# Optimization experiments

Hardware: AMD Instinct MI355X
Metric: run time of the kernel (lower is better)

The kernel has to match this reference:

```python
import jax, jax.numpy as jnp
import numpy as np

N, E, IN, H, C = 100_000, 1_600_000, 128, 4, 32  # nodes, edges, in_dim, heads, per-head channels
HC = H * C
SLOPE = 0.2  # negative_slope


def setup_inputs() -> dict:
    key = jax.random.key(0)
    ks = jax.random.split(key, 20)
    rn = lambda k, shape, s=0.05: jax.random.normal(k, shape, jnp.float32) * s
    inp = {
        'x': rn(ks[0], (N, IN), 1.0),
        'edge_index': jax.random.randint(ks[1], (2, E), 0, N),
    }
    for i in range(3):
        din = IN if i == 0 else HC
        inp[f'W{i}'] = rn(ks[2 + 4 * i], (din, HC))
        inp[f'as{i}'] = rn(ks[3 + 4 * i], (H, C))
        inp[f'ad{i}'] = rn(ks[4 + 4 * i], (H, C))
        inp[f'b{i}'] = jnp.zeros((HC,), jnp.float32)
    inp['llW'] = rn(ks[14], (HC, HC))
    inp['llb'] = jnp.zeros((HC,), jnp.float32)
    inp['opW'] = rn(ks[15], (3 * HC, C))  # concat_dim=384 -> out_dim=32
    inp['opb'] = jnp.zeros((C,), jnp.float32)
    return inp


def gat_layer(h, src, dst, W, a_s, a_d, b):
    # PyG GATConv with concat=True, add_self_loops=False, edge_dim=None, eval-mode dropout
    xh = (h @ W).reshape(-1, H, C)                        # [N,H,C]
    e_src = (xh * a_s).sum(-1)                            # [N,H]
    e_dst = (xh * a_d).sum(-1)                            # [N,H]
    e = jax.nn.leaky_relu(e_src[src] + e_dst[dst], SLOPE)  # [E,H]
    emax = jax.ops.segment_max(e, dst, num_segments=N)    # segment softmax over dst
    ee = jnp.exp(e - emax[dst])
    denom = jax.ops.segment_sum(ee, dst, num_segments=N)
    alpha = ee / denom[dst]                               # [E,H]
    out = jax.ops.segment_sum(xh[src] * alpha[:, :, None], dst, num_segments=N)  # [N,H,C]
    return out.reshape(-1, HC) + b


def reference(x, edge_index, W0, as0, ad0, b0, W1, as1, ad1, b1, W2, as2, ad2, b2, llW, llb, opW, opb):
    src, dst = edge_index[0], edge_index[1]
    # layer 0 (no residual at layer 0)
    h0 = gat_layer(x, src, dst, W0, as0, ad0, b0)
    # layer 1: residual
    h1 = gat_layer(h0, src, dst, W1, as1, ad1, b1) + h0
    # layer 2: residual through last_linear
    h2 = gat_layer(h1, src, dst, W2, as2, ad2, b2) + (h1 @ llW + llb)
    # encoder head: concat hidden list, project
    h = jnp.concatenate([h0, h1, h2], axis=-1)  # [N, 384]
    return h @ opW + opb                         # [N, 32]
```

## Files before the change

### kernel.cpp

```cpp
#include <hip/hip_runtime.h>
#include <hip/hip_bf16.h>

#define NN  100000
#define NE  1600000
#define NH4 400000
#define NHC 12800000
#define NBLK 391
#define SC_CHUNK 2048
#define SC_NCHUNK ((NE + SC_CHUNK - 1) / SC_CHUNK)

typedef __attribute__((ext_vector_type(8))) short bf16x8;
typedef __attribute__((ext_vector_type(4))) float f32x4;

__device__ __forceinline__ ushort f2bf(float f) {
  uint u = __float_as_uint(f);
  u += 0x7fff + ((u >> 16) & 1);
  return (ushort)(u >> 16);
}
__device__ __forceinline__ uint pack2(float a, float b) {
  return (uint)f2bf(a) | ((uint)f2bf(b) << 16);
}
__device__ __forceinline__ float blo(uint u) { return __uint_as_float(u << 16); }
__device__ __forceinline__ float bhi(uint u) { return __uint_as_float(u & 0xffff0000u); }

__device__ __forceinline__ void stage_A_bf16(const uint* __restrict__ Ab, int row0,
                                             uint* __restrict__ As, int tid) {
  const uint4* __restrict__ Ag = (const uint4*)(Ab + (size_t)row0 * 64);
#pragma unroll
  for (int i = 0; i < 4; i++) {
    const int idx = tid + 512 * i;
    const int r = idx >> 4, c4 = idx & 15;
    uint4 v = make_uint4(0u, 0u, 0u, 0u);
    if (row0 + r < NN) v = Ag[idx];
    const uint off = (uint)(r * 64 + c4 * 4) ^ (uint)((r & 7) << 2);
    *(uint4*)&As[off] = v;
  }
}
__device__ __forceinline__ void stage_A_f32(const float* __restrict__ Af, int row0,
                                            uint* __restrict__ As, int tid) {
  const float4* __restrict__ Ag = (const float4*)(Af + (size_t)row0 * 128);
#pragma unroll
  for (int i = 0; i < 8; i++) {
    const int idx = tid + 512 * i;
    const int r = idx >> 5, k4 = idx & 31;
    float4 a = make_float4(0.f, 0.f, 0.f, 0.f);
    if (row0 + r < NN) a = Ag[idx];
    uint2 p;
    p.x = pack2(a.x, a.y);
    p.y = pack2(a.z, a.w);
    const uint off = (uint)(r * 64 + k4 * 2) ^ (uint)((r & 7) << 2);
    *(uint2*)&As[off] = p;
  }
}
__device__ __forceinline__ void stage_W(const float* __restrict__ W,
                                        uint* __restrict__ Wt, int tid) {
#pragma unroll
  for (int i = 0; i < 4; i++) {
    const int cid = tid + 512 * i;
    const int n = cid & 127;
    const int k8 = cid >> 7;
    float v[8];
#pragma unroll
    for (int j = 0; j < 8; j++) v[j] = W[(size_t)(k8 * 8 + j) * 128 + n];
    uint4 p;
    p.x = pack2(v[0], v[1]);
    p.y = pack2(v[2], v[3]);
    p.z = pack2(v[4], v[5]);
    p.w = pack2(v[6], v[7]);
    const uint off = (uint)(n * 64 + k8 * 4) ^ (uint)((n & 7) << 2);
    *(uint4*)&Wt[off] = p;
  }
}
__device__ __forceinline__ void load_afrag(const uint* __restrict__ As, int w, int l,
                                           bf16x8* afrag) {
  const int lrow = l & 15, lku = (l >> 4) * 4;
#pragma unroll
  for (int kc = 0; kc < 4; kc++) {
    const int r = w * 16 + lrow;
    const uint off = (uint)(r * 64 + lku + kc * 16) ^ (uint)((r & 7) << 2);
    afrag[kc] = *(const bf16x8*)&As[off];
  }
}

__device__ __forceinline__ void mfma_write(const uint* __restrict__ Wt,
                                           const bf16x8* afrag, int row0, int w, int l,
                                           const float* __restrict__ bias1,
                                           const float* __restrict__ bias2,
                                           ushort* __restrict__ out,
                                           const float* __restrict__ as_,
                                           const float* __restrict__ ad_,
                                           float* __restrict__ es,
                                           float* __restrict__ ed) {
  const int lrow = l & 15, lku = (l >> 4) * 4;
  const int r0 = row0 + w * 16 + (l >> 4) * 4;
#pragma unroll
  for (int pair = 0; pair < 4; pair++) {
    float pa[4] = {0.f, 0.f, 0.f, 0.f};
    float qa[4] = {0.f, 0.f, 0.f, 0.f};
#pragma unroll
    for (int sub = 0; sub < 2; sub++) {
      const int nt = pair * 2 + sub;
      const int n = nt * 16 + lrow;
      f32x4 acc = {0.f, 0.f, 0.f, 0.f};
#pragma unroll
      for (int kc = 0; kc < 4; kc++) {
        const uint off = (uint)(n * 64 + lku + kc * 16) ^ (uint)((n & 7) << 2);
        const bf16x8 bfrag = *(const bf16x8*)&Wt[off];
        acc = __builtin_amdgcn_mfma_f32_16x16x32_bf16(afrag[kc], bfrag, acc, 0, 0, 0);
      }
      float badd = 0.f;
      if (bias1) badd += bias1[n];
      if (bias2) badd += bias2[n];
#pragma unroll
      for (int reg = 0; reg < 4; reg++) {
        const int r = r0 + reg;
        if (r < NN) out[(size_t)r * 128 + n] = f2bf(acc[reg] + badd);
      }
      if (as_) {
        const float av = as_[n], dv = ad_[n];
#pragma unroll
        for (int reg = 0; reg < 4; reg++) {
          pa[reg] = fmaf(acc[reg], av, pa[reg]);
          qa[reg] = fmaf(acc[reg], dv, qa[reg]);
        }
      }
    }
    if (as_) {
#pragma unroll
      for (int m = 1; m <= 8; m <<= 1) {
#pragma unroll
        for (int reg = 0; reg < 4; reg++) {
          pa[reg] += __shfl_xor(pa[reg], m);
          qa[reg] += __shfl_xor(qa[reg], m);
        }
      }
      if (lrow == 0) {
#pragma unroll
        for (int reg = 0; reg < 4; reg++) {
          const int r = r0 + reg;
          if (r < NN) {
            es[r * 4 + pair] = pa[reg];
            ed[r * 4 + pair] = qa[reg];
          }
        }
      }
    }
  }
}

template <bool ABF16>
__global__ __launch_bounds__(512) void gemm128_k(const void* __restrict__ Av,
                                                 const float* __restrict__ W,
                                                 ushort* __restrict__ out,
                                                 const float* __restrict__ bias1,
                                                 const float* __restrict__ bias2,
                                                 const float* __restrict__ as_,
                                                 const float* __restrict__ ad_,
                                                 float* __restrict__ es,
                                                 float* __restrict__ ed) {
  __shared__ uint As[128 * 64];
  __shared__ uint Wt[128 * 64];
  const int tid = threadIdx.x;
  const int row0 = blockIdx.x * 128;
  if constexpr (ABF16) stage_A_bf16((const uint*)Av, row0, As, tid);
  else                 stage_A_f32((const float*)Av, row0, As, tid);
  stage_W(W, Wt, tid);
  __syncthreads();
  const int w = tid >> 6, l = tid & 63;
  bf16x8 afrag[4];
  load_afrag(As, w, l, afrag);
  mfma_write(Wt, afrag, row0, w, l, bias1, bias2, out, as_, ad_, es, ed);
}

__global__ __launch_bounds__(512) void gemm2_k(const uint* __restrict__ Ab,
                                               const float* __restrict__ W1,
                                               const float* __restrict__ b1a,
                                               const float* __restrict__ b1b,
                                               ushort* __restrict__ out1,
                                               const float* __restrict__ W2,
                                               ushort* __restrict__ out2,
                                               const float* __restrict__ as_,
                                               const float* __restrict__ ad_,
                                               float* __restrict__ es,
                                               float* __restrict__ ed) {
  __shared__ uint As[128 * 64];
  __shared__ uint Wt[128 * 64];
  const int tid = threadIdx.x;
  const int row0 = blockIdx.x * 128;
  stage_A_bf16(Ab, row0, As, tid);
  stage_W(W1, Wt, tid);
  __syncthreads();
  const int w = tid >> 6, l = tid & 63;
  bf16x8 afrag[4];
  load_afrag(As, w, l, afrag);
  mfma_write(Wt, afrag, row0, w, l, b1a, b1b, out1, nullptr, nullptr, nullptr, nullptr);
  __syncthreads();
  stage_W(W2, Wt, tid);
  __syncthreads();
  mfma_write(Wt, afrag, row0, w, l, nullptr, nullptr, out2, as_, ad_, es, ed);
}

__global__ __launch_bounds__(256) void hist_k(const int* __restrict__ dst, int* __restrict__ counts) {
  const int g = blockIdx.x & 7;
  const int chunk = blockIdx.x >> 3;
  const int lo = g * (NN / 8);
  const int hi = lo + (NN / 8);
  const int e0 = chunk * SC_CHUNK;
  const int e1 = (e0 + SC_CHUNK < NE) ? e0 + SC_CHUNK : NE;
  for (int i = e0 + threadIdx.x; i < e1; i += 256) {
    const int d = dst[i];
    if (d >= lo && d < hi) atomicAdd(&counts[d], 1);
  }
}

__global__ __launch_bounds__(256) void scan_blk_k(const int* __restrict__ counts,
                                                  int* __restrict__ row_start,
                                                  int* __restrict__ blocksum) {
  __shared__ int sm[256];
  const int t = threadIdx.x;
  const int i = blockIdx.x * 256 + t;
  const int c = (i < NN) ? counts[i] : 0;
  sm[t] = c;
  __syncthreads();
#pragma unroll
  for (int off = 1; off < 256; off <<= 1) {
    const int v = (t >= off) ? sm[t - off] : 0;
    __syncthreads();
    sm[t] += v;
    __syncthreads();
  }
  if (i < NN) row_start[i] = sm[t] - c;
  if (t == 255) blocksum[blockIdx.x] = sm[255];
}

__global__ __launch_bounds__(512) void scan_top_k(const int* __restrict__ blocksum,
                                                  int* __restrict__ blockoff) {
  __shared__ int sm[512];
  const int t = threadIdx.x;
  const int c = (t < NBLK) ? blocksum[t] : 0;
  sm[t] = c;
  __syncthreads();
#pragma unroll
  for (int off = 1; off < 512; off <<= 1) {
    const int v = (t >= off) ? sm[t - off] : 0;
    __syncthreads();
    sm[t] += v;
    __syncthreads();
  }
  if (t < NBLK) blockoff[t] = sm[t] - c;
}

__global__ __launch_bounds__(256) void scan_fix_k(int* __restrict__ row_start,
                                                  const int* __restrict__ blockoff,
                                                  int* __restrict__ cursor) {
  const int i = blockIdx.x * 256 + threadIdx.x;
  if (i < NN) {
    const int v = row_start[i] + blockoff[blockIdx.x];
    row_start[i] = v;
    cursor[i] = v;
  }
  if (i == 0) row_start[NN] = NE;
}

__global__ __launch_bounds__(256) void scatter_k(const int* __restrict__ src,
                                                 const int* __restrict__ dst,
                                                 int* __restrict__ cursor,
                                                 int* __restrict__ csr_src) {
  const int g = blockIdx.x & 7;
  const int chunk = blockIdx.x >> 3;
  const int lo = g * (NN / 8);
  const int hi = lo + (NN / 8);
  const int e0 = chunk * SC_CHUNK;
  const int e1 = (e0 + SC_CHUNK < NE) ? e0 + SC_CHUNK : NE;
  for (int i = e0 + threadIdx.x; i < e1; i += 256) {
    const int d = dst[i];
    if (d >= lo && d < hi) {
      const int pos = atomicAdd(&cursor[d], 1);
      csr_src[pos] = src[i];
    }
  }
}

#define EDGE_BODY(sv)                                                      \
  {                                                                        \
    const int s_ = (sv);                                                   \
    float v_ = es[s_ * 4 + h] + edh;                                       \
    v_ = v_ > 0.f ? v_ : 0.2f * v_;                                        \
    const float w_ = __expf(v_);                                           \
    const uint m_ = xbf[(size_t)s_ * 64 + l];                              \
    den += w_;                                                             \
    ax = fmaf(w_, blo(m_), ax);                                            \
    ay = fmaf(w_, bhi(m_), ay);                                            \
  }

__global__ __launch_bounds__(256) void gat_agg_k(const int* __restrict__ row_start,
                                                 const int* __restrict__ csr_src,
                                                 const float* __restrict__ es,
                                                 const float* __restrict__ ed,
                                                 const uint* __restrict__ xbf,
                                                 const ushort* __restrict__ base,
                                                 const float* __restrict__ bias,
                                                 ushort* __restrict__ out) {
  const int wid = (blockIdx.x * 256 + threadIdx.x) >> 6;
  if (wid >= NN) return;
  const int l = threadIdx.x & 63;
  const int h = l >> 4;
  const float edh = ed[wid * 4 + h];
  const int beg = row_start[wid], end = row_start[wid + 1];
  float ax = 0.f, ay = 0.f, den = 0.f;
  int i = beg;
  for (; i + 8 <= end; i += 8) {
    const int s0 = csr_src[i],     s1 = csr_src[i + 1];
    const int s2 = csr_src[i + 2], s3 = csr_src[i + 3];
    const int s4 = csr_src[i + 4], s5 = csr_src[i + 5];
    const int s6 = csr_src[i + 6], s7 = csr_src[i + 7];
    EDGE_BODY(s0) EDGE_BODY(s1) EDGE_BODY(s2) EDGE_BODY(s3)
    EDGE_BODY(s4) EDGE_BODY(s5) EDGE_BODY(s6) EDGE_BODY(s7)
  }
  for (; i + 4 <= end; i += 4) {
    const int s0 = csr_src[i],     s1 = csr_src[i + 1];
    const int s2 = csr_src[i + 2], s3 = csr_src[i + 3];
    EDGE_BODY(s0) EDGE_BODY(s1) EDGE_BODY(s2) EDGE_BODY(s3)
  }
  for (; i < end; i++) EDGE_BODY(csr_src[i]);

  const float inv = den > 0.f ? 1.f / den : 0.f;
  float rx = ax * inv, ry = ay * inv;
  const size_t o = (size_t)wid * 64 + l;
  if (base) {
    const uint b = ((const uint*)base)[o];
    rx += blo(b); ry += bhi(b);
  }
  if (bias) { rx += bias[l * 2]; ry += bias[l * 2 + 1]; }
  ((uint*)out)[o] = pack2(rx, ry);
}

__global__ __launch_bounds__(512) void out_proj_k(const uint* __restrict__ h0,
                                                  const uint* __restrict__ h1,
                                                  const uint* __restrict__ h2,
                                                  const float* __restrict__ opW,
                                                  const float* __restrict__ opb,
                                                  float* __restrict__ out) {
  __shared__ uint As[128 * 64];
  __shared__ uint Wt[32 * 192];
  const int tid = threadIdx.x;
  const int row0 = blockIdx.x * 128;

#pragma unroll
  for (int i = 0; i < 3; i++) {
    const int cid = tid + 512 * i;
    const int n = cid & 31;
    const int k8 = cid >> 5;
    float v[8];
#pragma unroll
    for (int j = 0; j < 8; j++) v[j] = opW[(size_t)(k8 * 8 + j) * 32 + n];
    uint4 p;
    p.x = pack2(v[0], v[1]);
    p.y = pack2(v[2], v[3]);
    p.z = pack2(v[4], v[5]);
    p.w = pack2(v[6], v[7]);
    const uint off = (uint)(n * 192 + k8 * 4) ^ (uint)((n & 7) << 2);
    *(uint4*)&Wt[off] = p;
  }

  const int w = tid >> 6, l = tid & 63;
  const int lrow = l & 15, lku = (l >> 4) * 4;
  f32x4 acc0 = {0.f, 0.f, 0.f, 0.f};
  f32x4 acc1 = {0.f, 0.f, 0.f, 0.f};
  const uint* __restrict__ hs[3] = {h0, h1, h2};

  for (int seg = 0; seg < 3; seg++) {
    __syncthreads();
    stage_A_bf16(hs[seg], row0, As, tid);
    __syncthreads();
    bf16x8 afrag[4];
    load_afrag(As, w, l, afrag);
#pragma unroll
    for (int kc = 0; kc < 4; kc++) {
      const int n0 = lrow, n1 = 16 + lrow;
      const uint off0 = (uint)(n0 * 192 + seg * 64 + lku + kc * 16) ^ (uint)((n0 & 7) << 2);
      const uint off1 = (uint)(n1 * 192 + seg * 64 + lku + kc * 16) ^ (uint)((n1 & 7) << 2);
      const bf16x8 b0 = *(const bf16x8*)&Wt[off0];
      const bf16x8 b1 = *(const bf16x8*)&Wt[off1];
      acc0 = __builtin_amdgcn_mfma_f32_16x16x32_bf16(afrag[kc], b0, acc0, 0, 0, 0);
      acc1 = __builtin_amdgcn_mfma_f32_16x16x32_bf16(afrag[kc], b1, acc1, 0, 0, 0);
    }
  }

  const int r0 = row0 + w * 16 + (l >> 4) * 4;
  const float ba = opb[lrow], bb = opb[16 + lrow];
#pragma unroll
  for (int reg = 0; reg < 4; reg++) {
    const int r = r0 + reg;
    if (r < NN) {
      out[(size_t)r * 32 + lrow]      = acc0[reg] + ba;
      out[(size_t)r * 32 + 16 + lrow] = acc1[reg] + bb;
    }
  }
}

extern "C" void kernel_launch(void* const* d_in, const int* in_sizes, int n_in,
                              void* d_out, int out_size, void* d_ws, size_t ws_size,
                              hipStream_t stream) {
  (void)in_sizes; (void)n_in; (void)out_size; (void)ws_size;
  const float* x  = (const float*)d_in[0];
  const int*   ei = (const int*)d_in[1];
  const int*  src = ei;
  const int*  dst = ei + NE;
  const float *W0 = (const float*)d_in[2],  *as0 = (const float*)d_in[3],
              *ad0 = (const float*)d_in[4], *b0 = (const float*)d_in[5];
  const float *W1 = (const float*)d_in[6],  *as1 = (const float*)d_in[7],
              *ad1 = (const float*)d_in[8], *b1 = (const float*)d_in[9];
  const float *W2 = (const float*)d_in[10], *as2 = (const float*)d_in[11],
              *ad2 = (const float*)d_in[12], *b2 = (const float*)d_in[13];
  const float *llW = (const float*)d_in[14], *llb = (const float*)d_in[15];
  const float *opW = (const float*)d_in[16], *opb = (const float*)d_in[17];

  char* w = (char*)d_ws;
  ushort* h0b = (ushort*)w; w += (size_t)NHC * 2;
  ushort* h1b = (ushort*)w; w += (size_t)NHC * 2;
  ushort* h2b = (ushort*)w; w += (size_t)NHC * 2;
  uint*   xbf = (uint*)w;   w += (size_t)NHC * 2;
  float*  es  = (float*)w;  w += (size_t)NH4 * 4;
  float*  ed  = (float*)w;  w += (size_t)NH4 * 4;
  int* row_start = (int*)w; w += (size_t)(NN + 1) * 4;
  int* cursor    = (int*)w; w += (size_t)NN * 4;
  int* counts    = (int*)w; w += (size_t)NN * 4;
  int* csr_src   = (int*)w; w += (size_t)NE * 4;
  int* blocksum  = (int*)w; w += (size_t)NBLK * 4;
  int* blockoff  = (int*)w;

  const dim3 blk(256);
  hipMemsetAsync(counts, 0, (size_t)NN * 4, stream);
  hist_k<<<SC_NCHUNK * 8, blk, 0, stream>>>(dst, counts);
  scan_blk_k<<<NBLK, blk, 0, stream>>>(counts, row_start, blocksum);
  scan_top_k<<<1, 512, 0, stream>>>(blocksum, blockoff);
  scan_fix_k<<<NBLK, blk, 0, stream>>>(row_start, blockoff, cursor);
  scatter_k<<<SC_NCHUNK * 8, blk, 0, stream>>>(src, dst, cursor, csr_src);
  gemm128_k<false><<<782, 512, 0, stream>>>(x, W0, (ushort*)xbf, nullptr, nullptr,
                                            as0, ad0, es, ed);
  gat_agg_k<<<25000, blk, 0, stream>>>(row_start, csr_src, es, ed, xbf, nullptr, b0, h0b);
  gemm128_k<true><<<782, 512, 0, stream>>>(h0b, W1, (ushort*)xbf, nullptr, nullptr,
                                           as1, ad1, es, ed);
  gat_agg_k<<<25000, blk, 0, stream>>>(row_start, csr_src, es, ed, xbf, h0b, b1, h1b);
  gemm2_k<<<782, 512, 0, stream>>>((const uint*)h1b, llW, llb, b2, h2b, W2, (ushort*)xbf,
                                   as2, ad2, es, ed);
  gat_agg_k<<<25000, blk, 0, stream>>>(row_start, csr_src, es, ed, xbf, h2b, nullptr, h2b);
  out_proj_k<<<782, 512, 0, stream>>>((const uint*)h0b, (const uint*)h1b, (const uint*)h2b,
                                      opW, opb, (float*)d_out);
}
```

Before: 502.5 us.

## Fuse CSR scatter with layer-0 GEMM into one heterogeneous kernel launch

```diff
diff --git a/kernel.cpp b/kernel.cpp
--- a/kernel.cpp
+++ b/kernel.cpp
@@ -8,6 +8,9 @@
 #define NBLK 391
 #define SC_CHUNK 2048
 #define SC_NCHUNK ((NE + SC_CHUNK - 1) / SC_CHUNK)
+#define SG_CHUNK 4096
+#define SG_NCHUNK ((NE + SG_CHUNK - 1) / SG_CHUNK)
+#define NG_GEMM 782
 
 typedef __attribute__((ext_vector_type(8))) short bf16x8;
 typedef __attribute__((ext_vector_type(4))) float f32x4;
@@ -200,6 +203,51 @@
   mfma_write(Wt, afrag, row0, w, l, nullptr, nullptr, out2, as_, ad_, es, ed);
 }
 
+__global__ __launch_bounds__(512) void scatter_gemm0_k(const int* __restrict__ src,
+                                                       const int* __restrict__ dst,
+                                                       int* __restrict__ cursor,
+                                                       int* __restrict__ csr_src,
+                                                       const float* __restrict__ x,
+                                                       const float* __restrict__ W0,
+                                                       ushort* __restrict__ out,
+                                                       const float* __restrict__ as_,
+                                                       const float* __restrict__ ad_,
+                                                       float* __restrict__ es,
+                                                       float* __restrict__ ed) {
+  __shared__ uint As[128 * 64];
+  __shared__ uint Wt[128 * 64];
+  const int p = blockIdx.x / 40;
+  const int within = blockIdx.x % 40;
+  if (within < 8) {
+    const int gid = p * 8 + within;
+    if (gid >= NG_GEMM) return;
+    const int tid = threadIdx.x;
+    const int row0 = gid * 128;
+    stage_A_f32(x, row0, As, tid);
+    stage_W(W0, Wt, tid);
+    __syncthreads();
+    const int w = tid >> 6, l = tid & 63;
+    bf16x8 afrag[4];
+    load_afrag(As, w, l, afrag);
+    mfma_write(Wt, afrag, row0, w, l, nullptr, nullptr, out, as_, ad_, es, ed);
+  } else {
+    const int g = blockIdx.x & 7;
+    const int chunk = p * 4 + (within - 8) / 8;
+    if (chunk >= SG_NCHUNK) return;
+    const int lo = g * (NN / 8);
+    const int hi = lo + (NN / 8);
+    const int e0 = chunk * SG_CHUNK;
+    const int e1 = (e0 + SG_CHUNK < NE) ? e0 + SG_CHUNK : NE;
+    for (int i = e0 + threadIdx.x; i < e1; i += 512) {
+      const int d = dst[i];
+      if (d >= lo && d < hi) {
+        const int pos = atomicAdd(&cursor[d], 1);
+        csr_src[pos] = src[i];
+      }
+    }
+  }
+}
+
 __global__ __launch_bounds__(256) void hist_k(const int* __restrict__ dst, int* __restrict__ counts) {
   const int g = blockIdx.x & 7;
   const int chunk = blockIdx.x >> 3;
@@ -260,25 +308,6 @@
     cursor[i] = v;
   }
   if (i == 0) row_start[NN] = NE;
-}
-
-__global__ __launch_bounds__(256) void scatter_k(const int* __restrict__ src,
-                                                 const int* __restrict__ dst,
-                                                 int* __restrict__ cursor,
-                                                 int* __restrict__ csr_src) {
-  const int g = blockIdx.x & 7;
-  const int chunk = blockIdx.x >> 3;
-  const int lo = g * (NN / 8);
-  const int hi = lo + (NN / 8);
-  const int e0 = chunk * SC_CHUNK;
-  const int e1 = (e0 + SC_CHUNK < NE) ? e0 + SC_CHUNK : NE;
-  for (int i = e0 + threadIdx.x; i < e1; i += 256) {
-    const int d = dst[i];
-    if (d >= lo && d < hi) {
-      const int pos = atomicAdd(&cursor[d], 1);
-      csr_src[pos] = src[i];
-    }
-  }
 }
 
 #define EDGE_BODY(sv)                                                      \
@@ -436,9 +465,8 @@
   scan_blk_k<<<NBLK, blk, 0, stream>>>(counts, row_start, blocksum);
   scan_top_k<<<1, 512, 0, stream>>>(blocksum, blockoff);
   scan_fix_k<<<NBLK, blk, 0, stream>>>(row_start, blockoff, cursor);
-  scatter_k<<<SC_NCHUNK * 8, blk, 0, stream>>>(src, dst, cursor, csr_src);
-  gemm128_k<false><<<782, 512, 0, stream>>>(x, W0, (ushort*)xbf, nullptr, nullptr,
-                                            as0, ad0, es, ed);
+  scatter_gemm0_k<<<98 * 40, 512, 0, stream>>>(src, dst, cursor, csr_src,
+                                               x, W0, (ushort*)xbf, as0, ad0, es, ed);
   gat_agg_k<<<25000, blk, 0, stream>>>(row_start, csr_src, es, ed, xbf, nullptr, b0, h0b);
   gemm128_k<true><<<782, 512, 0, stream>>>(h0b, W1, (ushort*)xbf, nullptr, nullptr,
                                            as1, ad1, es, ed);
```

Measured after the change: 483.3 us, median of 2. -3.8%, faster.
